# Performance work log

Measured on AMD Instinct MI355X. Metric: run time of the kernel, lower is better.

Reference implementation:

```python
import jax, jax.numpy as jnp
import numpy as np

N, D, H, ED, E, T, L = 100000, 128, 128, 64, 500000, 2, 4


def _ln(x, g, b):
    m = jnp.mean(x, axis=-1, keepdims=True)
    v = jnp.var(x, axis=-1, keepdims=True)
    return (x - m) * jax.lax.rsqrt(v + 1e-5) * g + b


def _seg_softmax(s, seg, n):
    # softmax over edges grouped by segment id (torch scatter-softmax)
    m = jax.ops.segment_max(s, seg, num_segments=n)
    m = jnp.where(jnp.isfinite(m), m, 0.0)
    e = jnp.exp(s - m[seg])
    z = jax.ops.segment_sum(e, seg, num_segments=n)
    return e / (z[seg] + 1e-16)


def setup_inputs() -> dict:
    key = jax.random.key(0)
    ks = iter(jax.random.split(key, 64))
    p = lambda shape: jax.random.normal(next(ks), shape, dtype=jnp.float32) * 0.05
    inp = {
        'node_features': jax.random.normal(next(ks), (N, D), dtype=jnp.float32),
        'edge_features': jax.random.normal(next(ks), (T, E, ED), dtype=jnp.float32),
        'node_levels': jax.random.randint(next(ks), (N,), 0, L, dtype=jnp.int32),
        'edge_index': jax.random.randint(next(ks), (T, 2, E), 0, N, dtype=jnp.int32),
        # NodeLevelAttention params (stacked over T edge types)
        'nl_node_W': p((T, D, H)), 'nl_node_b': p((T, H)),
        'nl_edge_W': p((T, ED, H)), 'nl_edge_b': p((T, H)),
        'nl_att_W1': p((T, 3 * H, H)), 'nl_att_b1': p((T, H)),
        'nl_att_W2': p((T, H, 1)), 'nl_att_b2': p((T, 1)),
        'nl_out_W': p((T, H, H)), 'nl_out_b': p((T, H)),
        'nl_ln_g': jnp.ones((T, H), jnp.float32), 'nl_ln_b': jnp.zeros((T, H), jnp.float32),
        # EdgeLevelAttention params
        'el_att_W1': p((T, H, H)), 'el_att_b1': p((T, H)),
        'el_att_W2': p((T, H, 1)), 'el_att_b2': p((T, 1)),
        'el_out_W': p((H, H)), 'el_out_b': p((H,)),
        'el_ln_g': jnp.ones((H,), jnp.float32), 'el_ln_b': jnp.zeros((H,), jnp.float32),
        # HierarchicalAwarenessModule params
        'hl_proj_W': p((L, H, H)), 'hl_proj_b': p((L, H)),
        'hi_att_W1': p((2 * H, H)), 'hi_att_b1': p((H,)),
        'hi_att_W2': p((H, 1)), 'hi_att_b2': p((1,)),
        'hl_out_W': p((H, H)), 'hl_out_b': p((H,)),
        'hl_ln_g': jnp.ones((H,), jnp.float32), 'hl_ln_b': jnp.zeros((H,), jnp.float32),
    }
    return inp


def reference(node_features, edge_features, node_levels, edge_index,
              nl_node_W, nl_node_b, nl_edge_W, nl_edge_b,
              nl_att_W1, nl_att_b1, nl_att_W2, nl_att_b2,
              nl_out_W, nl_out_b, nl_ln_g, nl_ln_b,
              el_att_W1, el_att_b1, el_att_W2, el_att_b2,
              el_out_W, el_out_b, el_ln_g, el_ln_b,
              hl_proj_W, hl_proj_b, hi_att_W1, hi_att_b1,
              hi_att_W2, hi_att_b2, hl_out_W, hl_out_b, hl_ln_g, hl_ln_b):
    embs, scores = [], []
    for t in range(T):  # small fixed set of edge types
        h = node_features @ nl_node_W[t] + nl_node_b[t]              # [N,H]
        he = edge_features[t] @ nl_edge_W[t] + nl_edge_b[t]          # [E,H]
        s, d = edge_index[t, 0], edge_index[t, 1]
        cat = jnp.concatenate([h[s], h[d], he], axis=-1)             # [E,3H]
        a = jnp.tanh(cat @ nl_att_W1[t] + nl_att_b1[t]) @ nl_att_W2[t] + nl_att_b2[t]
        alpha = _seg_softmax(a[:, 0], s, N)[:, None]                 # softmax over out-edges of src
        agg = jax.ops.segment_sum(alpha * h[d], s, num_segments=N)  # [N,H]
        emb = jax.nn.relu(_ln(agg @ nl_out_W[t] + nl_out_b[t], nl_ln_g[t], nl_ln_b[t]))
        embs.append(emb)
        scores.append(jnp.tanh(emb @ el_att_W1[t] + el_att_b1[t]) @ el_att_W2[t] + el_att_b2[t])
    # EdgeLevelAttention: softmax over edge types per node
    w = jax.nn.softmax(jnp.concatenate(scores, axis=1), axis=1)      # [N,T]
    fused = sum(embs[t] * w[:, t:t + 1] for t in range(T))
    fused = jax.nn.relu(_ln(fused @ el_out_W + el_out_b, el_ln_g, el_ln_b))
    # HierarchicalAwarenessModule (vectorized form of the per-node loop)
    proj_all = jnp.einsum('nd,ldh->lnh', fused, hl_proj_W) + hl_proj_b[:, None, :]
    hf = proj_all[node_levels, jnp.arange(N)]                        # [N,H] level-specific projection
    counts = jax.ops.segment_sum(jnp.ones((N,), fused.dtype), node_levels, num_segments=L)
    lmean = jax.ops.segment_sum(hf, node_levels, num_segments=L) / jnp.maximum(counts, 1.0)[:, None]
    W1a, W1b = hi_att_W1[:H], hi_att_W1[H:]                          # split concat([h_i, mean_l]) matmul
    sc = jnp.tanh((hf @ W1a)[:, None, :] + (lmean @ W1b)[None, :, :] + hi_att_b1) @ hi_att_W2 + hi_att_b2
    aw = jax.nn.softmax(sc[..., 0], axis=1)                          # [N,L]
    enhanced = aw @ lmean                                            # [N,H]
    return jax.nn.relu(_ln(enhanced @ hl_out_W + hl_out_b, hl_ln_g, hl_ln_b))
```

## Files before the change

### kernel.cpp

```cpp
#include <hip/hip_runtime.h>
#include <math.h>

#define NN 100000
#define EE 500000
#define NH_C (NN * 128)
#define EBLK 32

typedef __attribute__((ext_vector_type(8))) short bf16x8;
typedef __attribute__((ext_vector_type(4))) float f32x4;
#define MFMA __builtin_amdgcn_mfma_f32_16x16x32_bf16

__device__ inline short f2bf(float x) {
    union { float f; unsigned u; } v; v.f = x;
    unsigned r = v.u + 0x7FFF + ((v.u >> 16) & 1);
    return (short)(r >> 16);
}
__device__ inline float bf2f(unsigned short h) {
    union { unsigned u; float f; } v; v.u = ((unsigned)h) << 16; return v.f;
}
__device__ inline float tanhf_fast(float x) {
    float e = __expf(2.0f * x);
    return 1.0f - 2.0f * __builtin_amdgcn_rcpf(e + 1.0f);
}

__device__ inline bf16x8 mk_hi(const float* p) {
    float4 a = *(const float4*)p, b = *(const float4*)(p + 4);
    float v[8] = {a.x, a.y, a.z, a.w, b.x, b.y, b.z, b.w};
    bf16x8 h;
#pragma unroll
    for (int i = 0; i < 8; i++) h[i] = f2bf(v[i]);
    return h;
}
__device__ inline bf16x8 mk_hi8(float4 a, float4 b) {
    float v[8] = {a.x, a.y, a.z, a.w, b.x, b.y, b.z, b.w};
    bf16x8 h;
#pragma unroll
    for (int i = 0; i < 8; i++) h[i] = f2bf(v[i]);
    return h;
}
__device__ inline void mk_split(const float* p, bf16x8& hi, bf16x8& lo) {
    float4 a = *(const float4*)p, b = *(const float4*)(p + 4);
    float v[8] = {a.x, a.y, a.z, a.w, b.x, b.y, b.z, b.w};
#pragma unroll
    for (int i = 0; i < 8; i++) {
        short h = f2bf(v[i]);
        hi[i] = h;
        lo[i] = f2bf(v[i] - bf2f((unsigned short)h));
    }
}

__global__ void k_zero(float* __restrict__ p, size_t n) {
    size_t i = (size_t)blockIdx.x * blockDim.x + threadIdx.x;
    size_t stride = (size_t)gridDim.x * blockDim.x;
    for (; i < n; i += stride) p[i] = 0.0f;
}
__global__ void k_zeroi(int* __restrict__ p, int n) {
    int i = blockIdx.x * blockDim.x + threadIdx.x;
    if (i < n) p[i] = 0;
}

__global__ __launch_bounds__(256) void k_hist2(const int* __restrict__ ei, int* __restrict__ deg2) {
    long g = (long)blockIdx.x * 256 + threadIdx.x;
    if (g < 2L * EE) {
        int t = g >= EE;
        long le = g - (long)t * EE;
        int s = ei[(size_t)t * 2 * EE + le];
        atomicAdd(&deg2[t * NN + s], 1);
    }
}
__global__ __launch_bounds__(512) void k_scan1(const int* __restrict__ deg,
                                               int* __restrict__ tmp, int* __restrict__ bsum) {
    __shared__ int sh[2][512];
    int b = blockIdx.x, tid = threadIdx.x;
    int i = b * 512 + tid;
    int v = (i < 2 * NN) ? deg[i] : 0;
    int cur = 0;
    sh[0][tid] = v;
    __syncthreads();
    for (int off = 1; off < 512; off <<= 1) {
        int nxt = cur ^ 1;
        int a = sh[cur][tid];
        if (tid >= off) a += sh[cur][tid - off];
        sh[nxt][tid] = a;
        __syncthreads();
        cur = nxt;
    }
    int incl = sh[cur][tid];
    if (i < 2 * NN) tmp[i] = incl;
    if (tid == 511) bsum[b] = incl;
}
__global__ __launch_bounds__(512) void k_scan2(const int* __restrict__ bsum, int* __restrict__ boff,
                                               int nB) {
    __shared__ int sh[2][512];
    int tid = threadIdx.x;
    int v = (tid < nB) ? bsum[tid] : 0;
    int cur = 0;
    sh[0][tid] = v;
    __syncthreads();
    for (int off = 1; off < 512; off <<= 1) {
        int nxt = cur ^ 1;
        int a = sh[cur][tid];
        if (tid >= off) a += sh[cur][tid - off];
        sh[nxt][tid] = a;
        __syncthreads();
        cur = nxt;
    }
    boff[tid] = sh[cur][tid] - v;
}
__global__ __launch_bounds__(512) void k_scan3(const int* __restrict__ deg,
                                               const int* __restrict__ tmp,
                                               const int* __restrict__ boff,
                                               int* __restrict__ rowptr, int* __restrict__ cursor) {
    int i = blockIdx.x * 512 + threadIdx.x;
    if (i < 2 * NN) {
        int r = tmp[i] - deg[i] + boff[blockIdx.x];
        rowptr[i] = r;
        cursor[i] = r;
    }
    if (i == 0) rowptr[2 * NN] = 2 * EE;
}
__global__ __launch_bounds__(256) void k_csr_scatter3(const int* __restrict__ ei,
                                                      int* __restrict__ cursor,
                                                      int* __restrict__ ceid,
                                                      int* __restrict__ cs,
                                                      int* __restrict__ cdst) {
    long g = (long)blockIdx.x * 256 + threadIdx.x;
    if (g < 2L * EE) {
        int t = g >= EE;
        long le = g - (long)t * EE;
        int s = ei[(size_t)t * 2 * EE + le];
        int d = ei[(size_t)t * 2 * EE + EE + le];
        int p = atomicAdd(&cursor[t * NN + s], 1);
        ceid[p] = (int)le;
        cs[p] = s;
        cdst[p] = d;
    }
}

__global__ __launch_bounds__(256) void k_count(const int* __restrict__ lev, int* __restrict__ cnt4) {
    __shared__ int lc[4];
    int tid = threadIdx.x;
    if (tid < 4) lc[tid] = 0;
    __syncthreads();
    for (long n = (long)blockIdx.x * 256 + tid; n < NN; n += (long)gridDim.x * 256)
        atomicAdd(&lc[lev[n]], 1);
    __syncthreads();
    if (tid < 4 && lc[tid]) atomicAdd(&cnt4[tid], lc[tid]);
}

__global__ void k_scan(const int* __restrict__ cnt4, int* __restrict__ off4,
                       int* __restrict__ boff5, int* __restrict__ cursor) {
    int o = 0, b = 0;
    for (int l = 0; l < 4; l++) {
        off4[l] = o; cursor[l] = o; boff5[l] = b;
        o += cnt4[l];
        b += (cnt4[l] + 15) >> 4;
    }
    boff5[4] = b;
}

__global__ __launch_bounds__(256) void k_scatter(const int* __restrict__ lev,
                                                 int* __restrict__ cursor,
                                                 int* __restrict__ perm) {
    __shared__ int lc[4], lb[4], lc2[4];
    int tid = threadIdx.x;
    if (tid < 4) { lc[tid] = 0; lc2[tid] = 0; }
    __syncthreads();
    int start = blockIdx.x * 800, end = start + 800;
    if (end > NN) end = NN;
    for (int n = start + tid; n < end; n += 256) atomicAdd(&lc[lev[n]], 1);
    __syncthreads();
    if (tid < 4 && lc[tid]) lb[tid] = atomicAdd(&cursor[tid], lc[tid]);
    __syncthreads();
    for (int n = start + tid; n < end; n += 256) {
        int l = lev[n];
        int p = atomicAdd(&lc2[l], 1);
        perm[lb[l] + p] = n;
    }
}

__global__ void k_prep_head2(const float* __restrict__ nlW, const float* __restrict__ nlb,
                             const float* __restrict__ aW1, const float* __restrict__ ab1,
                             const float* __restrict__ neW, const float* __restrict__ neb,
                             unsigned short* __restrict__ WhT2, unsigned short* __restrict__ WUT2,
                             unsigned short* __restrict__ WVT2, unsigned short* __restrict__ WET2,
                             float* __restrict__ beff2) {
    __shared__ float red[2];
    int t = blockIdx.x >> 7, j = blockIdx.x & 127, k = threadIdx.x;
    const float* Wn = nlW + (size_t)t * 16384;
    const float* bn = nlb + t * 128;
    const float* W1 = aW1 + (size_t)t * 384 * 128;
    const float* b1 = ab1 + t * 128;
    const float* We = neW + (size_t)t * 64 * 128;
    const float* be = neb + t * 128;
    WhT2[(size_t)t * 16384 + j * 128 + k] = (unsigned short)f2bf(Wn[k * 128 + j]);
    float su = 0.0f, sv = 0.0f;
    for (int m = 0; m < 128; m++) {
        float wkm = Wn[k * 128 + m];
        su = fmaf(wkm, W1[m * 128 + j], su);
        sv = fmaf(wkm, W1[(128 + m) * 128 + j], sv);
    }
    WUT2[(size_t)t * 16384 + j * 128 + k] = (unsigned short)f2bf(su);
    WVT2[(size_t)t * 16384 + j * 128 + k] = (unsigned short)f2bf(sv);
    if (k < 64) {
        float se = 0.0f;
        for (int m = 0; m < 128; m++) se = fmaf(We[k * 128 + m], W1[(256 + m) * 128 + j], se);
        WET2[(size_t)t * 8192 + j * 64 + k] = (unsigned short)f2bf(se);
    }
    float tk = bn[k] * (W1[k * 128 + j] + W1[(128 + k) * 128 + j]) + be[k] * W1[(256 + k) * 128 + j];
#pragma unroll
    for (int o = 32; o > 0; o >>= 1) tk += __shfl_down(tk, o);
    if ((k & 63) == 0) red[k >> 6] = tk;
    __syncthreads();
    if (k == 0) beff2[t * 128 + j] = b1[j] + red[0] + red[1];
}

struct WSrc { const float* s[6]; };
__global__ void k_prep_tail(WSrc ps, unsigned short* __restrict__ hi,
                            unsigned short* __restrict__ lo) {
    int m = blockIdx.x >> 6, blk = blockIdx.x & 63;
    const float* src = ps.s[m];
    unsigned short* h = hi + (size_t)m * 16384;
    unsigned short* l = lo + (size_t)m * 16384;
    int idx = blk * 256 + threadIdx.x;
    int k = idx >> 7, j = idx & 127;
    float v = src[idx];
    short hh = f2bf(v);
    h[j * 128 + k] = (unsigned short)hh;
    l[j * 128 + k] = (unsigned short)f2bf(v - bf2f((unsigned short)hh));
}

__global__ void k_prep_q(const float* __restrict__ hpW, const float* __restrict__ hpb,
                         const float* __restrict__ hW1a,
                         unsigned short* __restrict__ QWhi, unsigned short* __restrict__ QWlo,
                         float* __restrict__ qb) {
    int gidx = blockIdx.x * 256 + threadIdx.x;
    if (gidx < 4 * 16384) {
        int l = gidx >> 14, rem = gidx & 16383;
        int k = rem >> 7, j = rem & 127;
        const float* wr = hpW + (size_t)l * 16384 + (size_t)k * 128;
        float v = 0.0f;
        for (int m = 0; m < 128; m++) v = fmaf(wr[m], hW1a[m * 128 + j], v);
        short hh = f2bf(v);
        QWhi[(size_t)l * 16384 + j * 128 + k] = (unsigned short)hh;
        QWlo[(size_t)l * 16384 + j * 128 + k] = (unsigned short)f2bf(v - bf2f((unsigned short)hh));
    } else {
        int e = gidx - 4 * 16384;
        if (e < 512) {
            int l = e >> 7, j = e & 127;
            float v = 0.0f;
            for (int m = 0; m < 128; m++) v = fmaf(hpb[l * 128 + m], hW1a[m * 128 + j], v);
            qb[l * 128 + j] = v;
        }
    }
}

__global__ __launch_bounds__(256) void k_head2(const float* __restrict__ nf,
                                               const unsigned short* __restrict__ WhT2,
                                               const unsigned short* __restrict__ WUT2,
                                               const unsigned short* __restrict__ WVT2,
                                               const float* __restrict__ nlb,
                                               unsigned short* __restrict__ hbf2,
                                               unsigned short* __restrict__ U2,
                                               unsigned short* __restrict__ V2) {
    __shared__ __align__(16) float T[16][132];
    int tid = threadIdx.x;
    long row0 = (long)blockIdx.x * 16;
#pragma unroll
    for (int i = 0; i < 8; i++) {
        int idx = tid + i * 256;
        int r = idx >> 7, c = idx & 127;
        T[r][c] = nf[(row0 + r) * 128 + c];
    }
    __syncthreads();
    int w = tid >> 6, lane = tid & 63, lr = lane & 15, lg = lane >> 4;
    bf16x8 A[4];
#pragma unroll
    for (int k = 0; k < 4; k++) A[k] = mk_hi(&T[lr][k * 32 + lg * 8]);
    int col0 = w * 32 + lr, col1 = col0 + 16;
#pragma unroll
    for (int o = 0; o < 6; o++) {
        const unsigned short* wb =
            (o == 0) ? WhT2 : (o == 1) ? WUT2 : (o == 2) ? WVT2 :
            (o == 3) ? WhT2 + 16384 : (o == 4) ? WUT2 + 16384 : WVT2 + 16384;
        unsigned short* ob =
            (o == 0) ? hbf2 : (o == 1) ? U2 : (o == 2) ? V2 :
            (o == 3) ? hbf2 + NH_C : (o == 4) ? U2 + NH_C : V2 + NH_C;
        const unsigned short* w0 = wb + (size_t)col0 * 128 + lg * 8;
        const unsigned short* w1 = wb + (size_t)col1 * 128 + lg * 8;
        f32x4 a0 = {0.f, 0.f, 0.f, 0.f}, a1 = {0.f, 0.f, 0.f, 0.f};
#pragma unroll
        for (int k = 0; k < 4; k++) {
            a0 = MFMA(A[k], *(const bf16x8*)(w0 + k * 32), a0, 0, 0, 0);
            a1 = MFMA(A[k], *(const bf16x8*)(w1 + k * 32), a1, 0, 0, 0);
        }
        float bb0 = (o == 0) ? nlb[col0] : (o == 3) ? nlb[128 + col0] : 0.0f;
        float bb1 = (o == 0) ? nlb[col1] : (o == 3) ? nlb[128 + col1] : 0.0f;
        unsigned short* op = ob + (size_t)row0 * 128;
#pragma unroll
        for (int i = 0; i < 4; i++) {
            int r = lg * 4 + i;
            op[(size_t)r * 128 + col0] = (unsigned short)f2bf(a0[i] + bb0);
            op[(size_t)r * 128 + col1] = (unsigned short)f2bf(a1[i] + bb1);
        }
    }
}

__global__ __launch_bounds__(256) void k_edge5(const float* __restrict__ ef,
                                               const int* __restrict__ ceid,
                                               const int* __restrict__ cs,
                                               const int* __restrict__ cdst,
                                               const unsigned short* __restrict__ WET2,
                                               const unsigned short* __restrict__ U2,
                                               const unsigned short* __restrict__ V2,
                                               const float* __restrict__ beff2,
                                               const float* __restrict__ aW2,
                                               const float* __restrict__ ab2,
                                               float* __restrict__ ebuf2) {
    __shared__ __align__(16) float pre[EBLK][132];
    __shared__ float part[4][EBLK];
    __shared__ int eS[EBLK];
    int tid = threadIdx.x, w = tid >> 6, lane = tid & 63, lr = lane & 15, lg = lane >> 4;
    long p0 = (long)blockIdx.x * EBLK;
    int t = p0 >= (long)EE;
    const float* ef_t = ef + (size_t)t * EE * 64;
    const unsigned short* U_t = U2 + (size_t)t * NH_C;
    const unsigned short* V_t = V2 + (size_t)t * NH_C;
    {
        int eL = tid >> 3, sub = tid & 7;
        int uch = (sub + eL) & 7;
        long p = p0 + eL;
        int s = cs[p], d = cdst[p];
        const unsigned short* up = U_t + (size_t)s * 128 + uch * 16;
        const unsigned short* vp = V_t + (size_t)d * 128 + uch * 16;
        bf16x8 u0 = *(const bf16x8*)up, u1 = *(const bf16x8*)(up + 8);
        bf16x8 v0 = *(const bf16x8*)vp, v1 = *(const bf16x8*)(vp + 8);
        float tv[16];
#pragma unroll
        for (int i = 0; i < 8; i++)
            tv[i] = bf2f((unsigned short)u0[i]) + bf2f((unsigned short)v0[i]);
#pragma unroll
        for (int i = 0; i < 8; i++)
            tv[8 + i] = bf2f((unsigned short)u1[i]) + bf2f((unsigned short)v1[i]);
#pragma unroll
        for (int i = 0; i < 4; i++) {
            float4 f4 = {tv[4 * i], tv[4 * i + 1], tv[4 * i + 2], tv[4 * i + 3]};
            *(float4*)&pre[eL][uch * 16 + 4 * i] = f4;
        }
    }
    if (tid < EBLK) eS[tid] = ceid[p0 + tid];
    int col0 = w * 32 + lr, col1 = col0 + 16;
    bf16x8 B0[2], B1[2];
#pragma unroll
    for (int kk = 0; kk < 2; kk++) {
        B0[kk] = *(const bf16x8*)(WET2 + (size_t)t * 8192 + (size_t)col0 * 64 + kk * 32 + lg * 8);
        B1[kk] = *(const bf16x8*)(WET2 + (size_t)t * 8192 + (size_t)col1 * 64 + kk * 32 + lg * 8);
    }
    float be0 = beff2[t * 128 + col0], be1 = beff2[t * 128 + col1];
    float w20 = aW2[t * 128 + col0], w21 = aW2[t * 128 + col1];
    __syncthreads();
#pragma unroll
    for (int i16 = 0; i16 < 2; i16++) {
        int e = eS[i16 * 16 + lr];
        const float* ep = ef_t + (size_t)e * 64 + lg * 8;
        float4 L0 = *(const float4*)ep;
        float4 L1 = *(const float4*)(ep + 4);
        float4 L2 = *(const float4*)(ep + 32);
        float4 L3 = *(const float4*)(ep + 36);
        bf16x8 av0 = mk_hi8(L0, L1);
        bf16x8 av1 = mk_hi8(L2, L3);
        f32x4 a0 = {0.f, 0.f, 0.f, 0.f}, a1 = {0.f, 0.f, 0.f, 0.f};
        a0 = MFMA(av0, B0[0], a0, 0, 0, 0);
        a0 = MFMA(av1, B0[1], a0, 0, 0, 0);
        a1 = MFMA(av0, B1[0], a1, 0, 0, 0);
        a1 = MFMA(av1, B1[1], a1, 0, 0, 0);
#pragma unroll
        for (int q = 0; q < 4; q++) {
            int eL = i16 * 16 + lg * 4 + q;
            float v = tanhf_fast(a0[q] + pre[eL][col0] + be0) * w20 +
                      tanhf_fast(a1[q] + pre[eL][col1] + be1) * w21;
            v += __shfl_xor(v, 1);
            v += __shfl_xor(v, 2);
            v += __shfl_xor(v, 4);
            v += __shfl_xor(v, 8);
            if (lr == 0) part[w][eL] = v;
        }
    }
    __syncthreads();
    if (tid < EBLK) {
        float a = part[0][tid] + part[1][tid] + part[2][tid] + part[3][tid] + ab2[t];
        ebuf2[p0 + tid] = __expf(a);
    }
}

__global__ __launch_bounds__(256) void k_tailA2b(const int* __restrict__ rowptr2,
                                                 const int* __restrict__ cdst,
                                                 const float* __restrict__ ebufC,
                                                 const unsigned short* __restrict__ hbf2,
                                                 const unsigned short* __restrict__ twhi,
                                                 const unsigned short* __restrict__ twlo,
                                                 const float* __restrict__ ob,
                                                 const float* __restrict__ lng,
                                                 const float* __restrict__ lnb,
                                                 const float* __restrict__ eb1,
                                                 const float* __restrict__ eW2,
                                                 const float* __restrict__ eb2,
                                                 float* __restrict__ emb0,
                                                 float* __restrict__ emb1,
                                                 float* __restrict__ scores, int NBn) {
    __shared__ __align__(16) float T[16][132];
    __shared__ __align__(16) float T2[16][132];
    __shared__ float mu16[16], rs16[16], part[4][16];
    int tid = threadIdx.x;
    int t = blockIdx.x >= NBn;
    int bi = blockIdx.x - t * NBn;
    long row0 = (long)bi * 16;
    const int* rowp = rowptr2 + (size_t)t * NN;
    const unsigned short* hbf_t = hbf2 + (size_t)t * NH_C;
    const unsigned short* Whi = twhi + (size_t)t * 16384;
    const unsigned short* Wlo = twlo + (size_t)t * 16384;
    const unsigned short* Shi = twhi + (size_t)(2 + t) * 16384;
    const float* ob_t = ob + t * 128;
    const float* g_t = lng + t * 128;
    const float* bln_t = lnb + t * 128;
    const float* sb1 = eb1 + t * 128;
    const float* sW2 = eW2 + t * 128;
    float* emb = t ? emb1 : emb0;
    {
        int r16 = tid >> 4, sub = tid & 15;
        long n = row0 + r16;
        int p0 = rowp[n], p1 = rowp[n + 1];
        float acc[8] = {0, 0, 0, 0, 0, 0, 0, 0};
        float sev = 0.0f;
        int p = p0;
        for (; p + 4 <= p1; p += 4) {
            int d0 = cdst[p], d1 = cdst[p + 1], d2 = cdst[p + 2], d3 = cdst[p + 3];
            float ev0 = ebufC[p], ev1 = ebufC[p + 1];
            float ev2 = ebufC[p + 2], ev3 = ebufC[p + 3];
            bf16x8 h0 = *(const bf16x8*)(hbf_t + (size_t)d0 * 128 + sub * 8);
            bf16x8 h1 = *(const bf16x8*)(hbf_t + (size_t)d1 * 128 + sub * 8);
            bf16x8 h2 = *(const bf16x8*)(hbf_t + (size_t)d2 * 128 + sub * 8);
            bf16x8 h3 = *(const bf16x8*)(hbf_t + (size_t)d3 * 128 + sub * 8);
            sev += ev0 + ev1 + ev2 + ev3;
#pragma unroll
            for (int i = 0; i < 8; i++) {
                acc[i] = fmaf(ev0, bf2f((unsigned short)h0[i]), acc[i]);
                acc[i] = fmaf(ev1, bf2f((unsigned short)h1[i]), acc[i]);
                acc[i] = fmaf(ev2, bf2f((unsigned short)h2[i]), acc[i]);
                acc[i] = fmaf(ev3, bf2f((unsigned short)h3[i]), acc[i]);
            }
        }
        for (; p < p1; p++) {
            int d = cdst[p];
            float ev = ebufC[p];
            bf16x8 hv = *(const bf16x8*)(hbf_t + (size_t)d * 128 + sub * 8);
            sev += ev;
#pragma unroll
            for (int i = 0; i < 8; i++) acc[i] = fmaf(ev, bf2f((unsigned short)hv[i]), acc[i]);
        }
        float inv = 1.0f / (sev + 1e-16f);
#pragma unroll
        for (int i = 0; i < 8; i++) T[r16][sub * 8 + i] = acc[i] * inv;
    }
    __syncthreads();
    int w = tid >> 6, lane = tid & 63, lr = lane & 15, lg = lane >> 4;
    int col0 = w * 32 + lr, col1 = col0 + 16;
    int j = tid & 127, half = tid >> 7;
    {
        bf16x8 ahi[4], alo[4];
#pragma unroll
        for (int k = 0; k < 4; k++) mk_split(&T[lr][k * 32 + lg * 8], ahi[k], alo[k]);
        const unsigned short* wh0 = Whi + (size_t)col0 * 128 + lg * 8;
        const unsigned short* wl0 = Wlo + (size_t)col0 * 128 + lg * 8;
        const unsigned short* wh1 = Whi + (size_t)col1 * 128 + lg * 8;
        const unsigned short* wl1 = Wlo + (size_t)col1 * 128 + lg * 8;
        f32x4 a0 = {0.f, 0.f, 0.f, 0.f}, a1 = {0.f, 0.f, 0.f, 0.f};
#pragma unroll
        for (int k = 0; k < 4; k++) {
            bf16x8 bh = *(const bf16x8*)(wh0 + k * 32), bl = *(const bf16x8*)(wl0 + k * 32);
            a0 = MFMA(ahi[k], bh, a0, 0, 0, 0);
            a0 = MFMA(alo[k], bh, a0, 0, 0, 0);
            a0 = MFMA(ahi[k], bl, a0, 0, 0, 0);
            bh = *(const bf16x8*)(wh1 + k * 32); bl = *(const bf16x8*)(wl1 + k * 32);
            a1 = MFMA(ahi[k], bh, a1, 0, 0, 0);
            a1 = MFMA(alo[k], bh, a1, 0, 0, 0);
            a1 = MFMA(ahi[k], bl, a1, 0, 0, 0);
        }
#pragma unroll
        for (int i = 0; i < 4; i++) {
            int r = lg * 4 + i;
            T2[r][col0] = a0[i] + ob_t[col0];
            T2[r][col1] = a1[i] + ob_t[col1];
        }
    }
    __syncthreads();
    {
        int gr = tid >> 4, l16 = tid & 15;
        float sm = 0.0f, sq = 0.0f;
#pragma unroll
        for (int i = 0; i < 8; i++) {
            float v = T2[gr][l16 + 16 * i];
            sm += v; sq += v * v;
        }
#pragma unroll
        for (int m = 1; m < 16; m <<= 1) { sm += __shfl_xor(sm, m); sq += __shfl_xor(sq, m); }
        if (l16 == 0) {
            float mean = sm * (1.0f / 128.0f);
            float var = sq * (1.0f / 128.0f) - mean * mean;
            mu16[gr] = mean;
            rs16[gr] = rsqrtf(var + 1e-5f);
        }
    }
    __syncthreads();
    {
        float gj = g_t[j], bb = bln_t[j];
#pragma unroll
        for (int r = 0; r < 8; r++) {
            int rr = half * 8 + r;
            float v = fmaxf((T2[rr][j] - mu16[rr]) * rs16[rr] * gj + bb, 0.0f);
            emb[(row0 + rr) * 128 + j] = v;
            T2[rr][j] = v;
        }
    }
    __syncthreads();
    {
        bf16x8 ah[4];
#pragma unroll
        for (int k = 0; k < 4; k++) ah[k] = mk_hi(&T2[lr][k * 32 + lg * 8]);
        const unsigned short* wh0 = Shi + (size_t)col0 * 128 + lg * 8;
        const unsigned short* wh1 = Shi + (size_t)col1 * 128 + lg * 8;
        f32x4 a0 = {0.f, 0.f, 0.f, 0.f}, a1 = {0.f, 0.f, 0.f, 0.f};
#pragma unroll
        for (int k = 0; k < 4; k++) {
            a0 = MFMA(ah[k], *(const bf16x8*)(wh0 + k * 32), a0, 0, 0, 0);
            a1 = MFMA(ah[k], *(const bf16x8*)(wh1 + k * 32), a1, 0, 0, 0);
        }
        float b0 = sb1[col0], b1v = sb1[col1], w20 = sW2[col0], w21 = sW2[col1];
#pragma unroll
// ... 293 lines not shown
            T2[r][col1] = a1[i] + hob[col1];
        }
    }
    __syncthreads();
    {
        int gr = tid >> 4, l16 = tid & 15;
        float sm = 0.0f, sq = 0.0f;
#pragma unroll
        for (int i = 0; i < 8; i++) {
            float v = T2[gr][l16 + 16 * i];
            sm += v; sq += v * v;
        }
#pragma unroll
        for (int m = 1; m < 16; m <<= 1) { sm += __shfl_xor(sm, m); sq += __shfl_xor(sq, m); }
        if (l16 == 0) {
            float mean = sm * (1.0f / 128.0f);
            float var = sq * (1.0f / 128.0f) - mean * mean;
            mu16[gr] = mean;
            rs16[gr] = rsqrtf(var + 1e-5f);
        }
    }
    __syncthreads();
    {
        float gj = hlg[j], bb = hlb[j];
#pragma unroll
        for (int r = 0; r < 8; r++) {
            int rr = half * 8 + r;
            float v = (T2[rr][j] - mu16[rr]) * rs16[rr] * gj + bb;
            out[(size_t)idx16[rr] * 128 + j] = fmaxf(v, 0.0f);
        }
    }
}

extern "C" void kernel_launch(void* const* d_in, const int* in_sizes, int n_in,
                              void* d_out, int out_size, void* d_ws, size_t ws_size,
                              hipStream_t stream) {
    const float* nf  = (const float*)d_in[0];
    const float* ef  = (const float*)d_in[1];
    const int*   lev = (const int*)d_in[2];
    const int*   ei  = (const int*)d_in[3];
    const float* nlW = (const float*)d_in[4];
    const float* nlb = (const float*)d_in[5];
    const float* neW = (const float*)d_in[6];
    const float* neb = (const float*)d_in[7];
    const float* aW1 = (const float*)d_in[8];
    const float* ab1 = (const float*)d_in[9];
    const float* aW2 = (const float*)d_in[10];
    const float* ab2 = (const float*)d_in[11];
    const float* oW  = (const float*)d_in[12];
    const float* ob  = (const float*)d_in[13];
    const float* lng = (const float*)d_in[14];
    const float* lnb = (const float*)d_in[15];
    const float* eW1 = (const float*)d_in[16];
    const float* eb1 = (const float*)d_in[17];
    const float* eW2 = (const float*)d_in[18];
    const float* eb2 = (const float*)d_in[19];
    const float* eoW = (const float*)d_in[20];
    const float* eob = (const float*)d_in[21];
    const float* elg = (const float*)d_in[22];
    const float* elb = (const float*)d_in[23];
    const float* hpW = (const float*)d_in[24];
    const float* hpb = (const float*)d_in[25];
    const float* hW1 = (const float*)d_in[26];
    const float* hb1 = (const float*)d_in[27];
    const float* hW2 = (const float*)d_in[28];
    const float* hb2 = (const float*)d_in[29];
    const float* hoW = (const float*)d_in[30];
    const float* hob = (const float*)d_in[31];
    const float* hlg = (const float*)d_in[32];
    const float* hlb = (const float*)d_in[33];

    float* ws = (float*)d_ws;
    size_t NH = (size_t)NN * 128;
    float* fused2 = ws;
    float* emb0   = fused2 + NH;
    float* emb1   = emb0 + NH;
    float* ebuf2  = emb1 + NH;
    float* scores = ebuf2 + 2 * (size_t)EE;
    float* beff2  = scores + (size_t)2 * NN;
    float* fsum   = beff2 + 256;
    float* lmean  = fsum + 512;
    float* lmw    = lmean + 512;
    float* qb     = lmw + 512;
    unsigned short* U2    = (unsigned short*)(qb + 512);
    unsigned short* V2    = U2 + 2 * NH;
    unsigned short* hbf2  = V2 + 2 * NH;
    unsigned short* WhT2  = hbf2 + 2 * NH;
    unsigned short* WUT2  = WhT2 + 2 * 16384;
    unsigned short* WVT2  = WUT2 + 2 * 16384;
    unsigned short* WET2  = WVT2 + 2 * 16384;
    unsigned short* twhi  = WET2 + 2 * 8192;
    unsigned short* twlo  = twhi + 6 * 16384;
    unsigned short* QWhi  = twlo + 6 * 16384;
    unsigned short* QWlo  = QWhi + 4 * 16384;
    int* perm    = (int*)(QWlo + 4 * 16384);
    int* cnt4    = perm + NN;
    int* off4    = cnt4 + 4;
    int* boff5   = off4 + 4;
    int* cursorL = boff5 + 5;
    int* deg2    = cursorL + 4;
    int* rowptr2 = deg2 + 2 * NN;
    int* cursor2 = rowptr2 + 2 * NN + 1;
    int* stmp    = cursor2 + 2 * NN;
    int* sbsum   = stmp + 2 * NN;
    int* sboff   = sbsum + 512;
    int* ceid2   = sboff + 512;
    int* cs2     = ceid2 + 2 * EE;
    int* cdst2   = cs2 + 2 * EE;
    float* out = (float*)d_out;

    WSrc ps;
    ps.s[0] = oW;
    ps.s[1] = oW + 16384;
    ps.s[2] = eW1;
    ps.s[3] = eW1 + 16384;
    ps.s[4] = eoW;
    ps.s[5] = hoW;

    const int NB_N = NN / 16;
    const int SCB = (2 * NN + 511) / 512;

    k_zeroi<<<1, 4, 0, stream>>>(cnt4, 4);
    k_count<<<128, 256, 0, stream>>>(lev, cnt4);
    k_scan<<<1, 1, 0, stream>>>(cnt4, off4, boff5, cursorL);
    k_scatter<<<125, 256, 0, stream>>>(lev, cursorL, perm);

    k_prep_tail<<<6 * 64, 256, 0, stream>>>(ps, twhi, twlo);
    k_prep_q<<<258, 256, 0, stream>>>(hpW, hpb, hW1, QWhi, QWlo, qb);
    k_zero<<<1, 512, 0, stream>>>(fsum, (size_t)512);

    k_zeroi<<<(2 * NN + 255) / 256, 256, 0, stream>>>(deg2, 2 * NN);
    k_hist2<<<(2 * EE + 255) / 256, 256, 0, stream>>>(ei, deg2);
    k_scan1<<<SCB, 512, 0, stream>>>(deg2, stmp, sbsum);
    k_scan2<<<1, 512, 0, stream>>>(sbsum, sboff, SCB);
    k_scan3<<<SCB, 512, 0, stream>>>(deg2, stmp, sboff, rowptr2, cursor2);
    k_csr_scatter3<<<(2 * EE + 255) / 256, 256, 0, stream>>>(ei, cursor2, ceid2, cs2, cdst2);

    k_prep_head2<<<256, 128, 0, stream>>>(nlW, nlb, aW1, ab1, neW, neb,
                                          WhT2, WUT2, WVT2, WET2, beff2);
    k_head2<<<NB_N, 256, 0, stream>>>(nf, WhT2, WUT2, WVT2, nlb, hbf2, U2, V2);

    k_edge5<<<2 * EE / EBLK, 256, 0, stream>>>(ef, ceid2, cs2, cdst2, WET2, U2, V2,
                                               beff2, aW2, ab2, ebuf2);
    k_tailA2b<<<2 * NB_N, 256, 0, stream>>>(rowptr2, cdst2, ebuf2, hbf2, twhi, twlo,
                                            ob, lng, lnb, eb1, eW2, eb2,
                                            emb0, emb1, scores, NB_N);

    k_tailB1<<<NB_N, 256, 0, stream>>>(emb0, emb1, scores,
                                       twhi + (size_t)4 * 16384, twlo + (size_t)4 * 16384,
                                       eob, elg, elb, fused2);
    k_fsum<<<256, 256, 0, stream>>>(fused2, lev, fsum);
    k_fin2<<<4, 128, 0, stream>>>(fsum, cnt4, hpW, hpb, hW1 + 16384, hb1, lmean, lmw);
    k_tailCD2<<<NB_N + 4, 256, 0, stream>>>(fused2, perm, cnt4, off4, boff5,
                                            QWhi, QWlo, qb, lmw, lmean, hW2,
                                            twhi + (size_t)5 * 16384, twlo + (size_t)5 * 16384,
                                            hob, hlg, hlb, out);
}
```

Measured before the change: 942.8 us.

## Pre-convert edge features to bf16 in CSR order before edge kernel

Adds a pass that reads the fp32 edge features sequentially, converts them to bf16, and scatters them into CSR-sorted positions recorded by the CSR scatter kernel. The edge kernel then reads contiguous bf16 rows instead of gathering fp32 rows by edge id. This swaps a random 256B-per-edge gather for a streaming read plus a scattered 128B write and a contiguous 128B read, at the cost of one extra kernel launch and a 128MB intermediate buffer. The U/V gather swizzle is also reorganised into 8-element chunks.

```diff
diff --git a/kernel.cpp b/kernel.cpp
--- a/kernel.cpp
+++ b/kernel.cpp
@@ -25,13 +25,6 @@
 
 __device__ inline bf16x8 mk_hi(const float* p) {
     float4 a = *(const float4*)p, b = *(const float4*)(p + 4);
-    float v[8] = {a.x, a.y, a.z, a.w, b.x, b.y, b.z, b.w};
-    bf16x8 h;
-#pragma unroll
-    for (int i = 0; i < 8; i++) h[i] = f2bf(v[i]);
-    return h;
-}
-__device__ inline bf16x8 mk_hi8(float4 a, float4 b) {
     float v[8] = {a.x, a.y, a.z, a.w, b.x, b.y, b.z, b.w};
     bf16x8 h;
 #pragma unroll
@@ -119,9 +112,9 @@
     }
     if (i == 0) rowptr[2 * NN] = 2 * EE;
 }
-__global__ __launch_bounds__(256) void k_csr_scatter3(const int* __restrict__ ei,
+__global__ __launch_bounds__(256) void k_csr_scatter4(const int* __restrict__ ei,
                                                       int* __restrict__ cursor,
-                                                      int* __restrict__ ceid,
+                                                      int* __restrict__ epos,
                                                       int* __restrict__ cs,
                                                       int* __restrict__ cdst) {
     long g = (long)blockIdx.x * 256 + threadIdx.x;
@@ -131,10 +124,27 @@
         int s = ei[(size_t)t * 2 * EE + le];
         int d = ei[(size_t)t * 2 * EE + EE + le];
         int p = atomicAdd(&cursor[t * NN + s], 1);
-        ceid[p] = (int)le;
+        epos[g] = p;
         cs[p] = s;
         cdst[p] = d;
     }
+}
+
+__global__ __launch_bounds__(256) void k_efcvt(const float* __restrict__ ef,
+                                               const int* __restrict__ epos,
+                                               unsigned short* __restrict__ ebfC) {
+    long gid = (long)blockIdx.x * 256 + threadIdx.x;
+    if (gid >= 2L * EE * 8) return;
+    long e = gid >> 3;
+    int part = (int)(gid & 7);
+    const float* sp = ef + e * 64 + part * 8;
+    f32x4 a = __builtin_nontemporal_load((const f32x4*)sp);
+    f32x4 b = __builtin_nontemporal_load((const f32x4*)(sp + 4));
+    bf16x8 h;
+    h[0] = f2bf(a[0]); h[1] = f2bf(a[1]); h[2] = f2bf(a[2]); h[3] = f2bf(a[3]);
+    h[4] = f2bf(b[0]); h[5] = f2bf(b[1]); h[6] = f2bf(b[2]); h[7] = f2bf(b[3]);
+    long p = epos[e];
+    __builtin_nontemporal_store(h, (bf16x8*)(ebfC + p * 64 + part * 8));
 }
 
 __global__ __launch_bounds__(256) void k_count(const int* __restrict__ lev, int* __restrict__ cnt4) {
@@ -306,49 +316,44 @@
     }
 }
 
-__global__ __launch_bounds__(256) void k_edge5(const float* __restrict__ ef,
-                                               const int* __restrict__ ceid,
-                                               const int* __restrict__ cs,
-                                               const int* __restrict__ cdst,
-                                               const unsigned short* __restrict__ WET2,
-                                               const unsigned short* __restrict__ U2,
-                                               const unsigned short* __restrict__ V2,
-                                               const float* __restrict__ beff2,
-                                               const float* __restrict__ aW2,
-                                               const float* __restrict__ ab2,
-                                               float* __restrict__ ebuf2) {
+__global__ __launch_bounds__(256) void k_edge5b(const unsigned short* __restrict__ ebfC,
+                                                const int* __restrict__ cs,
+                                                const int* __restrict__ cdst,
+                                                const unsigned short* __restrict__ WET2,
+                                                const unsigned short* __restrict__ U2,
+                                                const unsigned short* __restrict__ V2,
+                                                const float* __restrict__ beff2,
+                                                const float* __restrict__ aW2,
+                                                const float* __restrict__ ab2,
+                                                float* __restrict__ ebuf2) {
     __shared__ __align__(16) float pre[EBLK][132];
     __shared__ float part[4][EBLK];
-    __shared__ int eS[EBLK];
     int tid = threadIdx.x, w = tid >> 6, lane = tid & 63, lr = lane & 15, lg = lane >> 4;
     long p0 = (long)blockIdx.x * EBLK;
     int t = p0 >= (long)EE;
-    const float* ef_t = ef + (size_t)t * EE * 64;
     const unsigned short* U_t = U2 + (size_t)t * NH_C;
     const unsigned short* V_t = V2 + (size_t)t * NH_C;
     {
         int eL = tid >> 3, sub = tid & 7;
-        int uch = (sub + eL) & 7;
         long p = p0 + eL;
         int s = cs[p], d = cdst[p];
-        const unsigned short* up = U_t + (size_t)s * 128 + uch * 16;
-        const unsigned short* vp = V_t + (size_t)d * 128 + uch * 16;
-        bf16x8 u0 = *(const bf16x8*)up, u1 = *(const bf16x8*)(up + 8);
-        bf16x8 v0 = *(const bf16x8*)vp, v1 = *(const bf16x8*)(vp + 8);
-        float tv[16];
-#pragma unroll
-        for (int i = 0; i < 8; i++)
-            tv[i] = bf2f((unsigned short)u0[i]) + bf2f((unsigned short)v0[i]);
-#pragma unroll
-        for (int i = 0; i < 8; i++)
-            tv[8 + i] = bf2f((unsigned short)u1[i]) + bf2f((unsigned short)v1[i]);
-#pragma unroll
-        for (int i = 0; i < 4; i++) {
-            float4 f4 = {tv[4 * i], tv[4 * i + 1], tv[4 * i + 2], tv[4 * i + 3]};
-            *(float4*)&pre[eL][uch * 16 + 4 * i] = f4;
-        }
-    }
-    if (tid < EBLK) eS[tid] = ceid[p0 + tid];
+        const unsigned short* up = U_t + (size_t)s * 128;
+        const unsigned short* vp = V_t + (size_t)d * 128;
+#pragma unroll
+        for (int i = 0; i < 2; i++) {
+            int c8 = ((sub - eL) & 7) | (i << 3);
+            bf16x8 u = *(const bf16x8*)(up + c8 * 8);
+            bf16x8 v = *(const bf16x8*)(vp + c8 * 8);
+            float tv[8];
+#pragma unroll
+            for (int k = 0; k < 8; k++)
+                tv[k] = bf2f((unsigned short)u[k]) + bf2f((unsigned short)v[k]);
+            float4 f0 = {tv[0], tv[1], tv[2], tv[3]};
+            float4 f1 = {tv[4], tv[5], tv[6], tv[7]};
+            *(float4*)&pre[eL][c8 * 8] = f0;
+            *(float4*)&pre[eL][c8 * 8 + 4] = f1;
+        }
+    }
     int col0 = w * 32 + lr, col1 = col0 + 16;
     bf16x8 B0[2], B1[2];
 #pragma unroll
@@ -361,14 +366,10 @@
     __syncthreads();
 #pragma unroll
     for (int i16 = 0; i16 < 2; i16++) {
-        int e = eS[i16 * 16 + lr];
-        const float* ep = ef_t + (size_t)e * 64 + lg * 8;
-        float4 L0 = *(const float4*)ep;
-        float4 L1 = *(const float4*)(ep + 4);
-        float4 L2 = *(const float4*)(ep + 32);
-        float4 L3 = *(const float4*)(ep + 36);
-        bf16x8 av0 = mk_hi8(L0, L1);
-        bf16x8 av1 = mk_hi8(L2, L3);
+        long p = p0 + i16 * 16 + lr;
+        const unsigned short* ap = ebfC + p * 64 + lg * 8;
+        bf16x8 av0 = __builtin_nontemporal_load((const bf16x8*)ap);
+        bf16x8 av1 = __builtin_nontemporal_load((const bf16x8*)(ap + 32));
         f32x4 a0 = {0.f, 0.f, 0.f, 0.f}, a1 = {0.f, 0.f, 0.f, 0.f};
         a0 = MFMA(av0, B0[0], a0, 0, 0, 0);
         a0 = MFMA(av1, B0[1], a0, 0, 0, 0);
@@ -916,7 +917,8 @@
     unsigned short* U2    = (unsigned short*)(qb + 512);
     unsigned short* V2    = U2 + 2 * NH;
     unsigned short* hbf2  = V2 + 2 * NH;
-    unsigned short* WhT2  = hbf2 + 2 * NH;
+    unsigned short* ebfC  = hbf2 + 2 * NH;
+    unsigned short* WhT2  = ebfC + 2 * (size_t)EE * 64;
     unsigned short* WUT2  = WhT2 + 2 * 16384;
     unsigned short* WVT2  = WUT2 + 2 * 16384;
     unsigned short* WET2  = WVT2 + 2 * 16384;
@@ -935,8 +937,8 @@
     int* stmp    = cursor2 + 2 * NN;
     int* sbsum   = stmp + 2 * NN;
     int* sboff   = sbsum + 512;
-    int* ceid2   = sboff + 512;
-    int* cs2     = ceid2 + 2 * EE;
+    int* epos2   = sboff + 512;
+    int* cs2     = epos2 + 2 * EE;
     int* cdst2   = cs2 + 2 * EE;
     float* out = (float*)d_out;
 
@@ -965,14 +967,16 @@
     k_scan1<<<SCB, 512, 0, stream>>>(deg2, stmp, sbsum);
     k_scan2<<<1, 512, 0, stream>>>(sbsum, sboff, SCB);
     k_scan3<<<SCB, 512, 0, stream>>>(deg2, stmp, sboff, rowptr2, cursor2);
-    k_csr_scatter3<<<(2 * EE + 255) / 256, 256, 0, stream>>>(ei, cursor2, ceid2, cs2, cdst2);
+    k_csr_scatter4<<<(2 * EE + 255) / 256, 256, 0, stream>>>(ei, cursor2, epos2, cs2, cdst2);
+
+    k_efcvt<<<(int)((2L * EE * 8 + 255) / 256), 256, 0, stream>>>(ef, epos2, ebfC);
 
     k_prep_head2<<<256, 128, 0, stream>>>(nlW, nlb, aW1, ab1, neW, neb,
                                           WhT2, WUT2, WVT2, WET2, beff2);
     k_head2<<<NB_N, 256, 0, stream>>>(nf, WhT2, WUT2, WVT2, nlb, hbf2, U2, V2);
 
-    k_edge5<<<2 * EE / EBLK, 256, 0, stream>>>(ef, ceid2, cs2, cdst2, WET2, U2, V2,
-                                               beff2, aW2, ab2, ebuf2);
+    k_edge5b<<<2 * EE / EBLK, 256, 0, stream>>>(ebfC, cs2, cdst2, WET2, U2, V2,
+                                                beff2, aW2, ab2, ebuf2);
     k_tailA2b<<<2 * NB_N, 256, 0, stream>>>(rowptr2, cdst2, ebuf2, hbf2, twhi, twlo,
                                             ob, lng, lnb, eb1, eW2, eb2,
                                             emb0, emb1, scores, NB_N);
```

New measurement: 981.5 us. 4.1% more time.

## Fold node projection into output weight and aggregate raw bf16 node features

Applied to the files above, without the earlier changes.

The node projection W_node is folded algebraically into the output linear layer (W_node·W_out, with the node bias propagated into an effective output bias). The tail kernel then aggregates a single shared bf16 copy of the raw node features instead of per-type projected features h. This drops the h output from the head GEMM and halves the gather source footprint, since both edge types share one nfbf buffer. The cost is an extra conversion kernel and a small weight-fold prep kernel, plus a slight change in rounding order. The bias fold is exact only because the softmax weights sum to one or the bias is scaled by sev.

```diff
diff --git a/kernel.cpp b/kernel.cpp
--- a/kernel.cpp
+++ b/kernel.cpp
@@ -57,6 +57,19 @@
 __global__ void k_zeroi(int* __restrict__ p, int n) {
     int i = blockIdx.x * blockDim.x + threadIdx.x;
     if (i < n) p[i] = 0;
+}
+
+__global__ __launch_bounds__(256) void k_nfcvt(const float* __restrict__ nf,
+                                               unsigned short* __restrict__ nfbf) {
+    long gid = (long)blockIdx.x * 256 + threadIdx.x;
+    if (gid >= (long)NH_C / 8) return;
+    const float* sp = nf + gid * 8;
+    f32x4 a = *(const f32x4*)sp;
+    f32x4 b = *(const f32x4*)(sp + 4);
+    bf16x8 h;
+    h[0] = f2bf(a[0]); h[1] = f2bf(a[1]); h[2] = f2bf(a[2]); h[3] = f2bf(a[3]);
+    h[4] = f2bf(b[0]); h[5] = f2bf(b[1]); h[6] = f2bf(b[2]); h[7] = f2bf(b[3]);
+    *(bf16x8*)(nfbf + gid * 8) = h;
 }
 
 __global__ __launch_bounds__(256) void k_hist2(const int* __restrict__ ei, int* __restrict__ deg2) {
@@ -182,7 +195,7 @@
 __global__ void k_prep_head2(const float* __restrict__ nlW, const float* __restrict__ nlb,
                              const float* __restrict__ aW1, const float* __restrict__ ab1,
                              const float* __restrict__ neW, const float* __restrict__ neb,
-                             unsigned short* __restrict__ WhT2, unsigned short* __restrict__ WUT2,
+                             unsigned short* __restrict__ WUT2,
                              unsigned short* __restrict__ WVT2, unsigned short* __restrict__ WET2,
                              float* __restrict__ beff2) {
     __shared__ float red[2];
@@ -193,7 +206,6 @@
     const float* b1 = ab1 + t * 128;
     const float* We = neW + (size_t)t * 64 * 128;
     const float* be = neb + t * 128;
-    WhT2[(size_t)t * 16384 + j * 128 + k] = (unsigned short)f2bf(Wn[k * 128 + j]);
     float su = 0.0f, sv = 0.0f;
     for (int m = 0; m < 128; m++) {
         float wkm = Wn[k * 128 + m];
@@ -215,7 +227,7 @@
     if (k == 0) beff2[t * 128 + j] = b1[j] + red[0] + red[1];
 }
 
-struct WSrc { const float* s[6]; };
+struct WSrc { const float* s[4]; };
 __global__ void k_prep_tail(WSrc ps, unsigned short* __restrict__ hi,
                             unsigned short* __restrict__ lo) {
     int m = blockIdx.x >> 6, blk = blockIdx.x & 63;
@@ -228,6 +240,33 @@
     short hh = f2bf(v);
     h[j * 128 + k] = (unsigned short)hh;
     l[j * 128 + k] = (unsigned short)f2bf(v - bf2f((unsigned short)hh));
+}
+
+__global__ void k_prep_fold(const float* __restrict__ nlW, const float* __restrict__ nlb,
+                            const float* __restrict__ oW, const float* __restrict__ ob,
+                            unsigned short* __restrict__ foldhi, unsigned short* __restrict__ foldlo,
+                            float* __restrict__ obf) {
+    int gidx = blockIdx.x * 256 + threadIdx.x;
+    if (gidx < 2 * 16384) {
+        int t = gidx >> 14, rem = gidx & 16383;
+        int k = rem >> 7, j = rem & 127;
+        const float* wn = nlW + (size_t)t * 16384 + (size_t)k * 128;
+        const float* ow = oW + (size_t)t * 16384;
+        float v = 0.0f;
+        for (int m = 0; m < 128; m++) v = fmaf(wn[m], ow[m * 128 + j], v);
+        short hh = f2bf(v);
+        foldhi[(size_t)t * 16384 + j * 128 + k] = (unsigned short)hh;
+        foldlo[(size_t)t * 16384 + j * 128 + k] = (unsigned short)f2bf(v - bf2f((unsigned short)hh));
+    } else {
+        int e = gidx - 2 * 16384;
+        if (e < 256) {
+            int t = e >> 7, j = e & 127;
+            float v = ob[t * 128 + j];
+            for (int m = 0; m < 128; m++)
+                v = fmaf(nlb[t * 128 + m], oW[(size_t)t * 16384 + m * 128 + j], v);
+            obf[t * 128 + j] = v;
+        }
+    }
 }
 
 __global__ void k_prep_q(const float* __restrict__ hpW, const float* __restrict__ hpb,
@@ -255,14 +294,11 @@
     }
 }
 
-__global__ __launch_bounds__(256) void k_head2(const float* __restrict__ nf,
-                                               const unsigned short* __restrict__ WhT2,
-                                               const unsigned short* __restrict__ WUT2,
-                                               const unsigned short* __restrict__ WVT2,
-                                               const float* __restrict__ nlb,
-                                               unsigned short* __restrict__ hbf2,
-                                               unsigned short* __restrict__ U2,
-                                               unsigned short* __restrict__ V2) {
+__global__ __launch_bounds__(256) void k_head2b(const float* __restrict__ nf,
+                                                const unsigned short* __restrict__ WUT2,
+                                                const unsigned short* __restrict__ WVT2,
+                                                unsigned short* __restrict__ U2,
+                                                unsigned short* __restrict__ V2) {
     __shared__ __align__(16) float T[16][132];
     int tid = threadIdx.x;
     long row0 = (long)blockIdx.x * 16;
@@ -279,13 +315,10 @@
     for (int k = 0; k < 4; k++) A[k] = mk_hi(&T[lr][k * 32 + lg * 8]);
     int col0 = w * 32 + lr, col1 = col0 + 16;
 #pragma unroll
-    for (int o = 0; o < 6; o++) {
-        const unsigned short* wb =
-            (o == 0) ? WhT2 : (o == 1) ? WUT2 : (o == 2) ? WVT2 :
-            (o == 3) ? WhT2 + 16384 : (o == 4) ? WUT2 + 16384 : WVT2 + 16384;
-        unsigned short* ob =
-            (o == 0) ? hbf2 : (o == 1) ? U2 : (o == 2) ? V2 :
-            (o == 3) ? hbf2 + NH_C : (o == 4) ? U2 + NH_C : V2 + NH_C;
+    for (int o = 0; o < 4; o++) {
+        int t = o >> 1, uv = o & 1;
+        const unsigned short* wb = (uv ? WVT2 : WUT2) + (size_t)t * 16384;
+        unsigned short* ob = (uv ? V2 : U2) + (size_t)t * NH_C;
         const unsigned short* w0 = wb + (size_t)col0 * 128 + lg * 8;
         const unsigned short* w1 = wb + (size_t)col1 * 128 + lg * 8;
         f32x4 a0 = {0.f, 0.f, 0.f, 0.f}, a1 = {0.f, 0.f, 0.f, 0.f};
@@ -294,14 +327,12 @@
             a0 = MFMA(A[k], *(const bf16x8*)(w0 + k * 32), a0, 0, 0, 0);
             a1 = MFMA(A[k], *(const bf16x8*)(w1 + k * 32), a1, 0, 0, 0);
         }
-        float bb0 = (o == 0) ? nlb[col0] : (o == 3) ? nlb[128 + col0] : 0.0f;
-        float bb1 = (o == 0) ? nlb[col1] : (o == 3) ? nlb[128 + col1] : 0.0f;
         unsigned short* op = ob + (size_t)row0 * 128;
 #pragma unroll
         for (int i = 0; i < 4; i++) {
             int r = lg * 4 + i;
-            op[(size_t)r * 128 + col0] = (unsigned short)f2bf(a0[i] + bb0);
-            op[(size_t)r * 128 + col1] = (unsigned short)f2bf(a1[i] + bb1);
+            op[(size_t)r * 128 + col0] = (unsigned short)f2bf(a0[i]);
+            op[(size_t)r * 128 + col1] = (unsigned short)f2bf(a1[i]);
         }
     }
 }
@@ -393,13 +424,14 @@
     }
 }
 
-__global__ __launch_bounds__(256) void k_tailA2b(const int* __restrict__ rowptr2,
+__global__ __launch_bounds__(256) void k_tailA2c(const int* __restrict__ rowptr2,
                                                  const int* __restrict__ cdst,
                                                  const float* __restrict__ ebufC,
-                                                 const unsigned short* __restrict__ hbf2,
+                                                 const unsigned short* __restrict__ nfbf,
+                                                 const unsigned short* __restrict__ foldhi,
+                                                 const unsigned short* __restrict__ foldlo,
                                                  const unsigned short* __restrict__ twhi,
-                                                 const unsigned short* __restrict__ twlo,
-                                                 const float* __restrict__ ob,
+                                                 const float* __restrict__ obf,
                                                  const float* __restrict__ lng,
                                                  const float* __restrict__ lnb,
                                                  const float* __restrict__ eb1,
@@ -416,11 +448,10 @@
     int bi = blockIdx.x - t * NBn;
     long row0 = (long)bi * 16;
     const int* rowp = rowptr2 + (size_t)t * NN;
-    const unsigned short* hbf_t = hbf2 + (size_t)t * NH_C;
-    const unsigned short* Whi = twhi + (size_t)t * 16384;
-    const unsigned short* Wlo = twlo + (size_t)t * 16384;
-    const unsigned short* Shi = twhi + (size_t)(2 + t) * 16384;
-    const float* ob_t = ob + t * 128;
+    const unsigned short* Whi = foldhi + (size_t)t * 16384;
+    const unsigned short* Wlo = foldlo + (size_t)t * 16384;
+    const unsigned short* Shi = twhi + (size_t)t * 16384;
+    const float* ob_t = obf + t * 128;
     const float* g_t = lng + t * 128;
     const float* bln_t = lnb + t * 128;
     const float* sb1 = eb1 + t * 128;
@@ -437,10 +468,10 @@
             int d0 = cdst[p], d1 = cdst[p + 1], d2 = cdst[p + 2], d3 = cdst[p + 3];
             float ev0 = ebufC[p], ev1 = ebufC[p + 1];
             float ev2 = ebufC[p + 2], ev3 = ebufC[p + 3];
-            bf16x8 h0 = *(const bf16x8*)(hbf_t + (size_t)d0 * 128 + sub * 8);
-            bf16x8 h1 = *(const bf16x8*)(hbf_t + (size_t)d1 * 128 + sub * 8);
-            bf16x8 h2 = *(const bf16x8*)(hbf_t + (size_t)d2 * 128 + sub * 8);
-            bf16x8 h3 = *(const bf16x8*)(hbf_t + (size_t)d3 * 128 + sub * 8);
+            bf16x8 h0 = *(const bf16x8*)(nfbf + (size_t)d0 * 128 + sub * 8);
+            bf16x8 h1 = *(const bf16x8*)(nfbf + (size_t)d1 * 128 + sub * 8);
+            bf16x8 h2 = *(const bf16x8*)(nfbf + (size_t)d2 * 128 + sub * 8);
+            bf16x8 h3 = *(const bf16x8*)(nfbf + (size_t)d3 * 128 + sub * 8);
             sev += ev0 + ev1 + ev2 + ev3;
 #pragma unroll
             for (int i = 0; i < 8; i++) {
@@ -453,7 +484,7 @@
         for (; p < p1; p++) {
             int d = cdst[p];
             float ev = ebufC[p];
-            bf16x8 hv = *(const bf16x8*)(hbf_t + (size_t)d * 128 + sub * 8);
+            bf16x8 hv = *(const bf16x8*)(nfbf + (size_t)d * 128 + sub * 8);
             sev += ev;
 #pragma unroll
             for (int i = 0; i < 8; i++) acc[i] = fmaf(ev, bf2f((unsigned short)hv[i]), acc[i]);
@@ -913,16 +944,18 @@
     float* lmean  = fsum + 512;
     float* lmw    = lmean + 512;
     float* qb     = lmw + 512;
-    unsigned short* U2    = (unsigned short*)(qb + 512);
+    float* obf    = qb + 512;
+    unsigned short* U2    = (unsigned short*)(obf + 256);
     unsigned short* V2    = U2 + 2 * NH;
-    unsigned short* hbf2  = V2 + 2 * NH;
-    unsigned short* WhT2  = hbf2 + 2 * NH;
-    unsigned short* WUT2  = WhT2 + 2 * 16384;
+    unsigned short* nfbf  = V2 + 2 * NH;
+    unsigned short* WUT2  = nfbf + NH;
     unsigned short* WVT2  = WUT2 + 2 * 16384;
     unsigned short* WET2  = WVT2 + 2 * 16384;
     unsigned short* twhi  = WET2 + 2 * 8192;
-    unsigned short* twlo  = twhi + 6 * 16384;
-    unsigned short* QWhi  = twlo + 6 * 16384;
+    unsigned short* twlo  = twhi + 4 * 16384;
+    unsigned short* foldhi = twlo + 4 * 16384;
+    unsigned short* foldlo = foldhi + 2 * 16384;
+    unsigned short* QWhi  = foldlo + 2 * 16384;
     unsigned short* QWlo  = QWhi + 4 * 16384;
     int* perm    = (int*)(QWlo + 4 * 16384);
     int* cnt4    = perm + NN;
@@ -941,12 +974,10 @@
     float* out = (float*)d_out;
 
     WSrc ps;
-    ps.s[0] = oW;
-    ps.s[1] = oW + 16384;
-    ps.s[2] = eW1;
-    ps.s[3] = eW1 + 16384;
-    ps.s[4] = eoW;
-    ps.s[5] = hoW;
+    ps.s[0] = eW1;
+    ps.s[1] = eW1 + 16384;
+    ps.s[2] = eoW;
+    ps.s[3] = hoW;
 
     const int NB_N = NN / 16;
     const int SCB = (2 * NN + 511) / 512;
@@ -956,9 +987,12 @@
     k_scan<<<1, 1, 0, stream>>>(cnt4, off4, boff5, cursorL);
     k_scatter<<<125, 256, 0, stream>>>(lev, cursorL, perm);
 
-    k_prep_tail<<<6 * 64, 256, 0, stream>>>(ps, twhi, twlo);
+    k_prep_tail<<<4 * 64, 256, 0, stream>>>(ps, twhi, twlo);
+    k_prep_fold<<<129, 256, 0, stream>>>(nlW, nlb, oW, ob, foldhi, foldlo, obf);
     k_prep_q<<<258, 256, 0, stream>>>(hpW, hpb, hW1, QWhi, QWlo, qb);
     k_zero<<<1, 512, 0, stream>>>(fsum, (size_t)512);
+
+    k_nfcvt<<<NH_C / 8 / 256, 256, 0, stream>>>(nf, nfbf);
 
     k_zeroi<<<(2 * NN + 255) / 256, 256, 0, stream>>>(deg2, 2 * NN);
     k_hist2<<<(2 * EE + 255) / 256, 256, 0, stream>>>(ei, deg2);
@@ -968,22 +1002,23 @@
     k_csr_scatter3<<<(2 * EE + 255) / 256, 256, 0, stream>>>(ei, cursor2, ceid2, cs2, cdst2);
 
     k_prep_head2<<<256, 128, 0, stream>>>(nlW, nlb, aW1, ab1, neW, neb,
-                                          WhT2, WUT2, WVT2, WET2, beff2);
-    k_head2<<<NB_N, 256, 0, stream>>>(nf, WhT2, WUT2, WVT2, nlb, hbf2, U2, V2);
+                                          WUT2, WVT2, WET2, beff2);
+    k_head2b<<<NB_N, 256, 0, stream>>>(nf, WUT2, WVT2, U2, V2);
 
     k_edge5<<<2 * EE / EBLK, 256, 0, stream>>>(ef, ceid2, cs2, cdst2, WET2, U2, V2,
                                                beff2, aW2, ab2, ebuf2);
-    k_tailA2b<<<2 * NB_N, 256, 0, stream>>>(rowptr2, cdst2, ebuf2, hbf2, twhi, twlo,
-                                            ob, lng, lnb, eb1, eW2, eb2,
+    k_tailA2c<<<2 * NB_N, 256, 0, stream>>>(rowptr2, cdst2, ebuf2, nfbf,
+                                            foldhi, foldlo, twhi, obf,
+                                            lng, lnb, eb1, eW2, eb2,
                                             emb0, emb1, scores, NB_N);
 
     k_tailB1<<<NB_N, 256, 0, stream>>>(emb0, emb1, scores,
-                                       twhi + (size_t)4 * 16384, twlo + (size_t)4 * 16384,
+                                       twhi + (size_t)2 * 16384, twlo + (size_t)2 * 16384,
                                        eob, elg, elb, fused2);
     k_fsum<<<256, 256, 0, stream>>>(fused2, lev, fsum);
     k_fin2<<<4, 128, 0, stream>>>(fsum, cnt4, hpW, hpb, hW1 + 16384, hb1, lmean, lmw);
     k_tailCD2<<<NB_N + 4, 256, 0, stream>>>(fused2, perm, cnt4, off4, boff5,
                                             QWhi, QWlo, qb, lmw, lmean, hW2,
-                                            twhi + (size_t)5 * 16384, twlo + (size_t)5 * 16384,
+                                            twhi + (size_t)3 * 16384, twlo + (size_t)3 * 16384,
                                             hob, hlg, hlb, out);
 }
```

After: 905.8 us, median of 2. -3.9%, faster.
